# Kernel tuning notes

Hardware: AMD Instinct MI355X
Metric: run time of the kernel (lower is better)

The kernel has to match this reference:

```python
import jax, jax.numpy as jnp
import numpy as np

EMB = 128
HID = 64
B = 4096
H = 200


def setup_inputs() -> dict:
    key = jax.random.key(0)
    ks = jax.random.split(key, 9)
    historical_embs = jax.random.normal(ks[0], (B, H, EMB), dtype=jnp.float32)
    candidate_emb = jax.random.normal(ks[1], (B, EMB), dtype=jnp.float32)
    mask = jax.random.randint(ks[2], (B, H), 0, 2, dtype=jnp.int32)
    # attention_net params: Linear(2*EMB -> HID), Linear(HID -> HID//2), Linear(HID//2 -> 1)
    def init_linear(k, fan_in, fan_out):
        k1, k2 = jax.random.split(k)
        bound = 1.0 / np.sqrt(fan_in)
        W = jax.random.uniform(k1, (fan_in, fan_out), jnp.float32, -bound, bound)
        b = jax.random.uniform(k2, (fan_out,), jnp.float32, -bound, bound)
        return W, b
    W1, b1 = init_linear(ks[3], 2 * EMB, HID)
    W2, b2 = init_linear(ks[4], HID, HID // 2)
    W3, b3 = init_linear(ks[5], HID // 2, 1)
    return {
        "historical_embs": historical_embs,
        "candidate_emb": candidate_emb,
        "W1": W1, "b1": b1, "W2": W2, "b2": b2, "W3": W3, "b3": b3,
        "mask": mask,
    }


def reference(historical_embs, candidate_emb, W1, b1, W2, b2, W3, b3, mask):
    # [B, H, 2*EMB] concat of history and broadcast candidate
    num_history = historical_embs.shape[1]
    cand = jnp.broadcast_to(candidate_emb[:, None, :], historical_embs.shape)
    combined = jnp.concatenate([historical_embs, cand], axis=-1)
    h = jax.nn.relu(combined @ W1 + b1)          # [B, H, HID]
    h = jax.nn.relu(h @ W2 + b2)                 # [B, H, HID//2]
    scores = (h @ W3 + b3)[..., 0]               # [B, H]
    scores = scores + (1.0 - mask.astype(scores.dtype)) * -1e9
    attention_weights = jax.nn.softmax(scores, axis=1)  # [B, H]
    aggregated = jnp.einsum('bh,bhd->bd', attention_weights, historical_embs)
    return aggregated, attention_weights
```

## Files before the change

### kernel.cpp

```cpp
#include <hip/hip_runtime.h>

#define EMB  128
#define HID  64
#define NH   200
#define BT   256
#define LDH1 68

#define WS_FRAG_BYTES 32768

typedef _Float16 half_t;
typedef half_t half2v __attribute__((ext_vector_type(2)));
typedef half_t half4v __attribute__((ext_vector_type(4)));
typedef half_t half8v __attribute__((ext_vector_type(8)));
typedef float  f32x4  __attribute__((ext_vector_type(4)));

static __device__ __forceinline__ half8v cvt8(float4 a, float4 b) {
    half8v r;
    r[0] = (half_t)a.x; r[1] = (half_t)a.y; r[2] = (half_t)a.z; r[3] = (half_t)a.w;
    r[4] = (half_t)b.x; r[5] = (half_t)b.y; r[6] = (half_t)b.z; r[7] = (half_t)b.w;
    return r;
}

__global__ __launch_bounds__(BT) void precomp_kernel(
    const float* __restrict__ W1, const float* __restrict__ b1,
    const float* __restrict__ W2, const float* __restrict__ cand,
    half8v* __restrict__ frag_ws, float* __restrict__ c1_ws, int nblk_c1)
{
    const int tid = threadIdx.x;
    if ((int)blockIdx.x == nblk_c1) {
        const int lane = tid & 63, wid = tid >> 6;
        const int c16 = lane & 15, quad = lane >> 4;
        #pragma unroll
        for (int ks = 0; ks < 4; ++ks) {
            half8v f;
            #pragma unroll
            for (int j = 0; j < 8; ++j)
                f[j] = (half_t)W1[(ks * 32 + quad * 8 + j) * HID + wid * 16 + c16];
            frag_ws[(wid * 4 + ks) * 64 + lane] = f;
        }
        if (wid == 0) {
            #pragma unroll
            for (int nt = 0; nt < 2; ++nt)
                #pragma unroll
                for (int ks = 0; ks < 2; ++ks) {
                    half8v f;
                    #pragma unroll
                    for (int j = 0; j < 8; ++j)
                        f[j] = (half_t)W2[(ks * 32 + quad * 8 + j) * (HID / 2) + nt * 16 + c16];
                    frag_ws[1024 + (nt * 2 + ks) * 64 + lane] = f;
                }
        }
    } else {
        __shared__ float W1b_s[EMB * HID];
        __shared__ float cand_s[4 * EMB];
        const int b0 = blockIdx.x * 4;
        {
            const float4* src = (const float4*)(W1 + EMB * HID);
            float4* dst = (float4*)W1b_s;
            for (int i = tid; i < EMB * HID / 4; i += BT) dst[i] = src[i];
            const float4* csrc = (const float4*)(cand + (size_t)b0 * EMB);
            float4* cdst = (float4*)cand_s;
            for (int i = tid; i < EMB; i += BT) cdst[i] = csrc[i];
        }
        __syncthreads();
        const int bl = tid >> 6, j = tid & 63;
        float acc = b1[j];
        #pragma unroll 8
        for (int k = 0; k < EMB; ++k)
            acc = fmaf(cand_s[bl * EMB + k], W1b_s[k * HID + j], acc);
        c1_ws[(size_t)(b0 + bl) * HID + j] = acc;
    }
}

__global__ __launch_bounds__(BT, 4) void attn_agg_kernel(
    const float* __restrict__ hist,
    const half8v* __restrict__ frag_ws,
    const float* __restrict__ c1_ws,
    const float* __restrict__ b2,
    const float* __restrict__ W3,
    const int*   __restrict__ mask,
    float* __restrict__ out_agg,
    float* __restrict__ out_attn)
{
    __shared__ __align__(16) half_t H1_s[NH * LDH1];
    __shared__ float attn_s[NH];
    __shared__ float2 red_s[BT];

    const int b    = blockIdx.x;
    const int tid  = threadIdx.x;
    const int lane = tid & 63;
    const int wid  = tid >> 6;
    const int c16  = lane & 15;
    const int quad = lane >> 4;

    const float* hb = hist + (size_t)b * (NH * EMB);

    half8v w1f[4];
    #pragma unroll
    for (int ks = 0; ks < 4; ++ks)
        w1f[ks] = frag_ws[(wid * 4 + ks) * 64 + lane];

    const float c1v = c1_ws[(size_t)b * HID + wid * 16 + c16];

    for (int t = 0; t < 13; ++t) {
        const int m0 = (t < 12) ? t * 16 : 184;
        const float* rp = hb + (m0 + c16) * EMB + quad * 8;
        float4 x0a = *(const float4*)(rp);
        float4 x0b = *(const float4*)(rp + 4);
        float4 x1a = *(const float4*)(rp + 32);
        float4 x1b = *(const float4*)(rp + 36);
        float4 x2a = *(const float4*)(rp + 64);
        float4 x2b = *(const float4*)(rp + 68);
        float4 x3a = *(const float4*)(rp + 96);
        float4 x3b = *(const float4*)(rp + 100);
        f32x4 acc = {0.f, 0.f, 0.f, 0.f};
        acc = __builtin_amdgcn_mfma_f32_16x16x32_f16(cvt8(x0a, x0b), w1f[0], acc, 0, 0, 0);
        acc = __builtin_amdgcn_mfma_f32_16x16x32_f16(cvt8(x1a, x1b), w1f[1], acc, 0, 0, 0);
        acc = __builtin_amdgcn_mfma_f32_16x16x32_f16(cvt8(x2a, x2b), w1f[2], acc, 0, 0, 0);
        acc = __builtin_amdgcn_mfma_f32_16x16x32_f16(cvt8(x3a, x3b), w1f[3], acc, 0, 0, 0);
        #pragma unroll
        for (int i = 0; i < 4; ++i) {
            int r = m0 + 4 * quad + i;
            H1_s[r * LDH1 + wid * 16 + c16] = (half_t)fmaxf(acc[i] + c1v, 0.f);
        }
    }
    __syncthreads();

    half8v w2f[2][2];
    w2f[0][0] = frag_ws[1024 + 0 * 64 + lane];
    w2f[0][1] = frag_ws[1024 + 1 * 64 + lane];
    w2f[1][0] = frag_ws[1024 + 2 * 64 + lane];
    w2f[1][1] = frag_ws[1024 + 3 * 64 + lane];
    const float w3a  = W3[c16];
    const float w3b  = W3[16 + c16];
    const float bb2a = b2[c16];
    const float bb2b = b2[16 + c16];

    for (int t = wid; t < 13; t += 4) {
        const int m0 = (t < 12) ? t * 16 : 184;
        const int row = m0 + c16;
        f32x4 acc0 = {0.f, 0.f, 0.f, 0.f};
        f32x4 acc1 = {0.f, 0.f, 0.f, 0.f};
        #pragma unroll
        for (int ks = 0; ks < 2; ++ks) {
            const half_t* ap = &H1_s[row * LDH1 + ks * 32 + quad * 8];
            half4v alo = *(const half4v*)ap;
            half4v ahi = *(const half4v*)(ap + 4);
            half8v a = __builtin_shufflevector(alo, ahi, 0, 1, 2, 3, 4, 5, 6, 7);
            acc0 = __builtin_amdgcn_mfma_f32_16x16x32_f16(a, w2f[0][ks], acc0, 0, 0, 0);
            acc1 = __builtin_amdgcn_mfma_f32_16x16x32_f16(a, w2f[1][ks], acc1, 0, 0, 0);
        }
        float sp[4];
        #pragma unroll
        for (int i = 0; i < 4; ++i)
            sp[i] = fmaxf(acc0[i] + bb2a, 0.f) * w3a + fmaxf(acc1[i] + bb2b, 0.f) * w3b;
        #pragma unroll
        for (int m = 1; m < 16; m <<= 1)
            #pragma unroll
            for (int i = 0; i < 4; ++i)
                sp[i] += __shfl_xor(sp[i], m, 64);
        if (c16 == 0) {
            const int lo = (t == 12) ? 192 : m0;
            #pragma unroll
            for (int i = 0; i < 4; ++i) {
                int r = m0 + 4 * quad + i;
                if (r >= lo) attn_s[r] = sp[i];
            }
        }
    }
    __syncthreads();

    if (tid < 64) {
        const int* mb = mask + (size_t)b * NH;
        float s0 = attn_s[tid]       + (1.f - (float)mb[tid])       * -1e9f;
        float s1 = attn_s[64 + tid]  + (1.f - (float)mb[64 + tid])  * -1e9f;
        float s2 = attn_s[128 + tid] + (1.f - (float)mb[128 + tid]) * -1e9f;
        float s3 = (tid < 8) ? attn_s[192 + tid] + (1.f - (float)mb[192 + tid]) * -1e9f : -1e30f;
        float m = fmaxf(fmaxf(s0, s1), fmaxf(s2, s3));
        #pragma unroll
        for (int off = 32; off; off >>= 1) m = fmaxf(m, __shfl_xor(m, off, 64));
        float e0 = __expf(s0 - m);
        float e1 = __expf(s1 - m);
        float e2 = __expf(s2 - m);
        float e3 = (tid < 8) ? __expf(s3 - m) : 0.f;
        float sum = e0 + e1 + e2 + e3;
        #pragma unroll
        for (int off = 32; off; off >>= 1) sum += __shfl_xor(sum, off, 64);
        float inv = 1.f / sum;
        e0 *= inv; e1 *= inv; e2 *= inv; e3 *= inv;
        attn_s[tid] = e0; attn_s[64 + tid] = e1; attn_s[128 + tid] = e2;
        if (tid < 8) attn_s[192 + tid] = e3;
        float* oa = out_attn + (size_t)b * NH;
        oa[tid] = e0; oa[64 + tid] = e1; oa[128 + tid] = e2;
        if (tid < 8) oa[192 + tid] = e3;
    }
    __syncthreads();

    {
        const int c = tid & 63;
        const int g = wid;
        float2 acc = make_float2(0.f, 0.f);
        const float* xp = hb + g * 50 * EMB + 2 * c;
        #pragma unroll 5
        for (int h = 0; h < 50; ++h) {
            float w = attn_s[g * 50 + h];
            float2 v = *(const float2*)(xp + (size_t)h * EMB);
            acc.x = fmaf(w, v.x, acc.x);
            acc.y = fmaf(w, v.y, acc.y);
        }
        red_s[tid] = acc;
        __syncthreads();
        if (tid < 64) {
            float2 r0 = red_s[tid], r1 = red_s[64 + tid], r2 = red_s[128 + tid], r3 = red_s[192 + tid];
            float2 o = make_float2(r0.x + r1.x + r2.x + r3.x,
                                   r0.y + r1.y + r2.y + r3.y);
            *(float2*)&out_agg[(size_t)b * EMB + tid * 2] = o;
        }
    }
}

extern "C" void kernel_launch(void* const* d_in, const int* in_sizes, int n_in,
                              void* d_out, int out_size, void* d_ws, size_t ws_size,
                              hipStream_t stream) {
    const float* hist = (const float*)d_in[0];
    const float* cand = (const float*)d_in[1];
    const float* W1   = (const float*)d_in[2];
    const float* b1   = (const float*)d_in[3];
    const float* W2   = (const float*)d_in[4];
    const float* b2   = (const float*)d_in[5];
    const float* W3   = (const float*)d_in[6];
    const int*   mask = (const int*)d_in[8];

    const int B = in_sizes[0] / (NH * EMB * 4);
    const int Brows = in_sizes[0] / (NH * EMB);
    (void)B;

    float* out_agg  = (float*)d_out;
    float* out_attn = out_agg + (size_t)Brows * EMB;

    half8v* frag_ws = (half8v*)d_ws;
    float*  c1_ws   = (float*)((char*)d_ws + WS_FRAG_BYTES);

    const int nblk_c1 = Brows / 4;
    precomp_kernel<<<nblk_c1 + 1, BT, 0, stream>>>(W1, b1, W2, cand, frag_ws, c1_ws, nblk_c1);
    attn_agg_kernel<<<Brows, BT, 0, stream>>>(hist, frag_ws, c1_ws, b2, W3, mask,
                                              out_agg, out_attn);
}
```

Before: 661.8 us.

## Split fused attention kernel into row-tiled scores kernel and softmax-aggregate kernel

```diff
diff --git a/kernel.cpp b/kernel.cpp
--- a/kernel.cpp
+++ b/kernel.cpp
@@ -4,22 +4,17 @@
 #define HID  64
 #define NH   200
 #define BT   256
+#define LDX  132
 #define LDH1 68
 
 #define WS_FRAG_BYTES 32768
+#define WS_C1_BYTES   (1u << 20)
 
 typedef _Float16 half_t;
 typedef half_t half2v __attribute__((ext_vector_type(2)));
 typedef half_t half4v __attribute__((ext_vector_type(4)));
 typedef half_t half8v __attribute__((ext_vector_type(8)));
 typedef float  f32x4  __attribute__((ext_vector_type(4)));
-
-static __device__ __forceinline__ half8v cvt8(float4 a, float4 b) {
-    half8v r;
-    r[0] = (half_t)a.x; r[1] = (half_t)a.y; r[2] = (half_t)a.z; r[3] = (half_t)a.w;
-    r[4] = (half_t)b.x; r[5] = (half_t)b.y; r[6] = (half_t)b.z; r[7] = (half_t)b.w;
-    return r;
-}
 
 __global__ __launch_bounds__(BT) void precomp_kernel(
     const float* __restrict__ W1, const float* __restrict__ b1,
@@ -72,72 +67,90 @@
     }
 }
 
-__global__ __launch_bounds__(BT, 4) void attn_agg_kernel(
+__global__ __launch_bounds__(BT, 4) void scores_kernel(
     const float* __restrict__ hist,
     const half8v* __restrict__ frag_ws,
     const float* __restrict__ c1_ws,
     const float* __restrict__ b2,
     const float* __restrict__ W3,
-    const int*   __restrict__ mask,
-    float* __restrict__ out_agg,
-    float* __restrict__ out_attn)
+    float* __restrict__ scores_ws)
 {
-    __shared__ __align__(16) half_t H1_s[NH * LDH1];
-    __shared__ float attn_s[NH];
-    __shared__ float2 red_s[BT];
-
-    const int b    = blockIdx.x;
+    __shared__ __align__(16) half_t X_s[64 * LDX];
+    __shared__ __align__(16) half_t H1_s[64 * LDH1];
+    __shared__ float c1a_s[HID], c1b_s[HID];
+
     const int tid  = threadIdx.x;
     const int lane = tid & 63;
     const int wid  = tid >> 6;
     const int c16  = lane & 15;
     const int quad = lane >> 4;
 
-    const float* hb = hist + (size_t)b * (NH * EMB);
+    const int r0  = blockIdx.x * 64;
+    const int b0r = r0 / 200;
+    const int b1r = (r0 + 63) / 200;
+    const int thr = (b0r + 1) * 200;
+
+    if (tid < HID)            c1a_s[tid]       = c1_ws[(size_t)b0r * HID + tid];
+    else if (tid < 2 * HID)   c1b_s[tid - HID] = c1_ws[(size_t)b1r * HID + (tid - HID)];
 
     half8v w1f[4];
     #pragma unroll
     for (int ks = 0; ks < 4; ++ks)
         w1f[ks] = frag_ws[(wid * 4 + ks) * 64 + lane];
 
-    const float c1v = c1_ws[(size_t)b * HID + wid * 16 + c16];
-
-    for (int t = 0; t < 13; ++t) {
-        const int m0 = (t < 12) ? t * 16 : 184;
-        const float* rp = hb + (m0 + c16) * EMB + quad * 8;
-        float4 x0a = *(const float4*)(rp);
-        float4 x0b = *(const float4*)(rp + 4);
-        float4 x1a = *(const float4*)(rp + 32);
-        float4 x1b = *(const float4*)(rp + 36);
-        float4 x2a = *(const float4*)(rp + 64);
-        float4 x2b = *(const float4*)(rp + 68);
-        float4 x3a = *(const float4*)(rp + 96);
-        float4 x3b = *(const float4*)(rp + 100);
-        f32x4 acc = {0.f, 0.f, 0.f, 0.f};
-        acc = __builtin_amdgcn_mfma_f32_16x16x32_f16(cvt8(x0a, x0b), w1f[0], acc, 0, 0, 0);
-        acc = __builtin_amdgcn_mfma_f32_16x16x32_f16(cvt8(x1a, x1b), w1f[1], acc, 0, 0, 0);
-        acc = __builtin_amdgcn_mfma_f32_16x16x32_f16(cvt8(x2a, x2b), w1f[2], acc, 0, 0, 0);
-        acc = __builtin_amdgcn_mfma_f32_16x16x32_f16(cvt8(x3a, x3b), w1f[3], acc, 0, 0, 0);
-        #pragma unroll
-        for (int i = 0; i < 4; ++i) {
-            int r = m0 + 4 * quad + i;
-            H1_s[r * LDH1 + wid * 16 + c16] = (half_t)fmaxf(acc[i] + c1v, 0.f);
+    {
+        const float4* src = (const float4*)(hist + (size_t)r0 * EMB);
+        #pragma unroll
+        for (int t = 0; t < 8; ++t) {
+            int i = t * BT + tid;
+            int h = i >> 5, c4 = i & 31;
+            float4 v = src[i];
+            half2v p0 = {(half_t)v.x, (half_t)v.y};
+            half2v p1 = {(half_t)v.z, (half_t)v.w};
+            *(half2v*)&X_s[h * LDX + c4 * 4]     = p0;
+            *(half2v*)&X_s[h * LDX + c4 * 4 + 2] = p1;
         }
     }
     __syncthreads();
 
-    half8v w2f[2][2];
-    w2f[0][0] = frag_ws[1024 + 0 * 64 + lane];
-    w2f[0][1] = frag_ws[1024 + 1 * 64 + lane];
-    w2f[1][0] = frag_ws[1024 + 2 * 64 + lane];
-    w2f[1][1] = frag_ws[1024 + 3 * 64 + lane];
-    const float w3a  = W3[c16];
-    const float w3b  = W3[16 + c16];
-    const float bb2a = b2[c16];
-    const float bb2b = b2[16 + c16];
-
-    for (int t = wid; t < 13; t += 4) {
-        const int m0 = (t < 12) ? t * 16 : 184;
+    {
+        const float c1va = c1a_s[wid * 16 + c16];
+        const float c1vb = c1b_s[wid * 16 + c16];
+        #pragma unroll
+        for (int t = 0; t < 4; ++t) {
+            const int m0 = t * 16;
+            const int row = m0 + c16;
+            f32x4 acc = {0.f, 0.f, 0.f, 0.f};
+            #pragma unroll
+            for (int ks = 0; ks < 4; ++ks) {
+                const half_t* ap = &X_s[row * LDX + ks * 32 + quad * 8];
+                half4v alo = *(const half4v*)ap;
+                half4v ahi = *(const half4v*)(ap + 4);
+                half8v a = __builtin_shufflevector(alo, ahi, 0, 1, 2, 3, 4, 5, 6, 7);
+                acc = __builtin_amdgcn_mfma_f32_16x16x32_f16(a, w1f[ks], acc, 0, 0, 0);
+            }
+            #pragma unroll
+            for (int i = 0; i < 4; ++i) {
+                int rr = m0 + 4 * quad + i;
+                float c1v = (r0 + rr < thr) ? c1va : c1vb;
+                H1_s[rr * LDH1 + wid * 16 + c16] = (half_t)fmaxf(acc[i] + c1v, 0.f);
+            }
+        }
+    }
+    __syncthreads();
+
+    {
+        half8v w2f[2][2];
+        w2f[0][0] = frag_ws[1024 + 0 * 64 + lane];
+        w2f[0][1] = frag_ws[1024 + 1 * 64 + lane];
+        w2f[1][0] = frag_ws[1024 + 2 * 64 + lane];
+        w2f[1][1] = frag_ws[1024 + 3 * 64 + lane];
+        const float w3a  = W3[c16];
+        const float w3b  = W3[16 + c16];
+        const float bb2a = b2[c16];
+        const float bb2b = b2[16 + c16];
+
+        const int m0 = wid * 16;
         const int row = m0 + c16;
         f32x4 acc0 = {0.f, 0.f, 0.f, 0.f};
         f32x4 acc1 = {0.f, 0.f, 0.f, 0.f};
@@ -160,22 +173,34 @@
             for (int i = 0; i < 4; ++i)
                 sp[i] += __shfl_xor(sp[i], m, 64);
         if (c16 == 0) {
-            const int lo = (t == 12) ? 192 : m0;
-            #pragma unroll
-            for (int i = 0; i < 4; ++i) {
-                int r = m0 + 4 * quad + i;
-                if (r >= lo) attn_s[r] = sp[i];
-            }
-        }
-    }
-    __syncthreads();
+            #pragma unroll
+            for (int i = 0; i < 4; ++i)
+                scores_ws[(size_t)r0 + m0 + 4 * quad + i] = sp[i];
+        }
+    }
+}
+
+__global__ __launch_bounds__(BT, 8) void softmax_agg_kernel(
+    const float* __restrict__ hist,
+    const float* __restrict__ scores_ws,
+    const int*   __restrict__ mask,
+    float* __restrict__ out_agg,
+    float* __restrict__ out_attn,
+    int Bn)
+{
+    __shared__ float attn_s[NH];
+    __shared__ __align__(16) f32x4 red_s[BT];
+
+    const int tid = threadIdx.x;
+    const int b = Bn - 1 - (int)blockIdx.x;
 
     if (tid < 64) {
+        const float* sc = scores_ws + (size_t)b * NH;
         const int* mb = mask + (size_t)b * NH;
-        float s0 = attn_s[tid]       + (1.f - (float)mb[tid])       * -1e9f;
-        float s1 = attn_s[64 + tid]  + (1.f - (float)mb[64 + tid])  * -1e9f;
-        float s2 = attn_s[128 + tid] + (1.f - (float)mb[128 + tid]) * -1e9f;
-        float s3 = (tid < 8) ? attn_s[192 + tid] + (1.f - (float)mb[192 + tid]) * -1e9f : -1e30f;
+        float s0 = sc[tid]       + (1.f - (float)mb[tid])       * -1e9f;
+        float s1 = sc[64 + tid]  + (1.f - (float)mb[64 + tid])  * -1e9f;
+        float s2 = sc[128 + tid] + (1.f - (float)mb[128 + tid]) * -1e9f;
+        float s3 = (tid < 8) ? sc[192 + tid] + (1.f - (float)mb[192 + tid]) * -1e9f : -1e30f;
         float m = fmaxf(fmaxf(s0, s1), fmaxf(s2, s3));
         #pragma unroll
         for (int off = 32; off; off >>= 1) m = fmaxf(m, __shfl_xor(m, off, 64));
@@ -197,24 +222,32 @@
     __syncthreads();
 
     {
-        const int c = tid & 63;
-        const int g = wid;
-        float2 acc = make_float2(0.f, 0.f);
-        const float* xp = hb + g * 50 * EMB + 2 * c;
+        const int c   = tid & 63;
+        const int g   = tid >> 6;
+        const int h2  = c >> 5;
+        const int c32 = c & 31;
+        const float4* hp = (const float4*)(hist + (size_t)b * NH * EMB);
+        f32x4 acc = {0.f, 0.f, 0.f, 0.f};
         #pragma unroll 5
-        for (int h = 0; h < 50; ++h) {
-            float w = attn_s[g * 50 + h];
-            float2 v = *(const float2*)(xp + (size_t)h * EMB);
-            acc.x = fmaf(w, v.x, acc.x);
-            acc.y = fmaf(w, v.y, acc.y);
+        for (int j = 0; j < 25; ++j) {
+            int h = g * 50 + 2 * j + h2;
+            float w = attn_s[h];
+            float4 v = hp[h * 32 + c32];
+            acc[0] = fmaf(w, v.x, acc[0]);
+            acc[1] = fmaf(w, v.y, acc[1]);
+            acc[2] = fmaf(w, v.z, acc[2]);
+            acc[3] = fmaf(w, v.w, acc[3]);
         }
         red_s[tid] = acc;
         __syncthreads();
-        if (tid < 64) {
-            float2 r0 = red_s[tid], r1 = red_s[64 + tid], r2 = red_s[128 + tid], r3 = red_s[192 + tid];
-            float2 o = make_float2(r0.x + r1.x + r2.x + r3.x,
-                                   r0.y + r1.y + r2.y + r3.y);
-            *(float2*)&out_agg[(size_t)b * EMB + tid * 2] = o;
+        if (tid < 32) {
+            f32x4 o = red_s[tid];
+            #pragma unroll
+            for (int k = 1; k < 8; ++k) {
+                f32x4 r = red_s[k * 32 + tid];
+                o[0] += r[0]; o[1] += r[1]; o[2] += r[2]; o[3] += r[3];
+            }
+            *(f32x4*)&out_agg[(size_t)b * EMB + tid * 4] = o;
         }
     }
 }
@@ -231,18 +264,21 @@
     const float* W3   = (const float*)d_in[6];
     const int*   mask = (const int*)d_in[8];
 
-    const int B = in_sizes[0] / (NH * EMB * 4);
     const int Brows = in_sizes[0] / (NH * EMB);
-    (void)B;
 
     float* out_agg  = (float*)d_out;
     float* out_attn = out_agg + (size_t)Brows * EMB;
 
-    half8v* frag_ws = (half8v*)d_ws;
-    float*  c1_ws   = (float*)((char*)d_ws + WS_FRAG_BYTES);
+    half8v* frag_ws   = (half8v*)d_ws;
+    float*  c1_ws     = (float*)((char*)d_ws + WS_FRAG_BYTES);
+    float*  scores_ws = (float*)((char*)d_ws + WS_FRAG_BYTES + WS_C1_BYTES);
 
     const int nblk_c1 = Brows / 4;
     precomp_kernel<<<nblk_c1 + 1, BT, 0, stream>>>(W1, b1, W2, cand, frag_ws, c1_ws, nblk_c1);
-    attn_agg_kernel<<<Brows, BT, 0, stream>>>(hist, frag_ws, c1_ws, b2, W3, mask,
-                                              out_agg, out_attn);
-}
+
+    const int nblk_scores = (Brows * NH) / 64;
+    scores_kernel<<<nblk_scores, BT, 0, stream>>>(hist, frag_ws, c1_ws, b2, W3, scores_ws);
+
+    softmax_agg_kernel<<<Brows, BT, 0, stream>>>(hist, scores_ws, mask,
+                                                 out_agg, out_attn, Brows);
+}
```

After: 622.6 us. 5.9% less time.
